# Optimization experiments

Measured on AMD Instinct MI355X. Metric: run time of the kernel, lower is better.

The kernel has to match this reference:

```python
import jax, jax.numpy as jnp
import numpy as np

B, T, C = 4, 2048, 768
H = 12
D = C // H  # head dim 64

def setup_inputs() -> dict:
    key = jax.random.key(0)
    ks = jax.random.split(key, 6)
    scale = 1.0 / np.sqrt(C)
    x = jax.random.normal(ks[0], (B, T, C), dtype=jnp.float32)
    attention_mask = jax.random.randint(ks[1], (B, T), 0, 2, dtype=jnp.int64)
    Wqkv = jax.random.normal(ks[2], (C, 3 * C), dtype=jnp.float32) * scale
    bqkv = jax.random.normal(ks[3], (3 * C,), dtype=jnp.float32) * 0.02
    Wo = jax.random.normal(ks[4], (C, C), dtype=jnp.float32) * scale
    bo = jax.random.normal(ks[5], (C,), dtype=jnp.float32) * 0.02
    return {"x": x, "attention_mask": attention_mask, "Wqkv": Wqkv,
            "bqkv": bqkv, "Wo": Wo, "bo": bo}

def reference(x, attention_mask, Wqkv, bqkv, Wo, bo):
    # fused QKV projection: [B,T,3C]
    qkv = jnp.einsum('btc,cd->btd', x, Wqkv) + bqkv
    q, k, v = jnp.split(qkv, 3, axis=-1)
    # reshape to [B,H,T,D]
    q = q.reshape(B, T, H, D).transpose(0, 2, 1, 3)
    k = k.reshape(B, T, H, D).transpose(0, 2, 1, 3)
    v = v.reshape(B, T, H, D).transpose(0, 2, 1, 3)
    # module quirk: True (attended) where attention_mask == 0
    keep = (attention_mask == 0)[:, None, None, :]  # [B,1,1,T]
    scores = jnp.einsum('bhqd,bhkd->bhqk', q, k) / np.sqrt(D)
    scores = jnp.where(keep, scores, jnp.finfo(scores.dtype).min)
    probs = jax.nn.softmax(scores, axis=-1)
    context = jnp.einsum('bhqk,bhkd->bhqd', probs, v)
    context = context.transpose(0, 2, 1, 3).reshape(B, T, C)
    return jnp.einsum('btc,cd->btd', context, Wo) + bo
```

## Files before the change

### kernel.cpp

```cpp
#include <hip/hip_runtime.h>
#include <stdint.h>

#define AS1 __attribute__((address_space(1)))
#define AS3 __attribute__((address_space(3)))

typedef _Float16 f16;
typedef _Float16 f16x8 __attribute__((ext_vector_type(8)));
typedef _Float16 f16x4 __attribute__((ext_vector_type(4)));
typedef _Float16 f16x2 __attribute__((ext_vector_type(2)));
typedef float    f32x4  __attribute__((ext_vector_type(4)));
typedef float    f32x16 __attribute__((ext_vector_type(16)));
typedef uint32_t u32x4  __attribute__((ext_vector_type(4)));
typedef uint32_t u32x2  __attribute__((ext_vector_type(2)));

#define B_  4
#define T_  2048
#define C_  768
#define H_  12
#define D_  64
#define M_  (B_*T_)
#define N1_ (3*C_)

__device__ __forceinline__ void g2l16(const void* g, void* l) {
  __builtin_amdgcn_global_load_lds((const AS1 void*)g, (AS3 void*)l, 16, 0, 0);
}

__device__ __forceinline__ f32x4 fzero4() { f32x4 z = {0.f, 0.f, 0.f, 0.f}; return z; }

__device__ __forceinline__ uint32_t pk_u32(float a, float b) {
  auto t = __builtin_amdgcn_cvt_pkrtz(a, b);
  return *(uint32_t*)&t;
}

__device__ __forceinline__ void pl32swap(uint32_t& d, uint32_t& s) {
  u32x2 r = __builtin_amdgcn_permlane32_swap(d, s, false, false);
  d = r[0]; s = r[1];
}

__global__ __launch_bounds__(256)
void prep_kernel(const float* __restrict__ Wqkv, f16* __restrict__ WqkvT,
                 const float* __restrict__ Wo, f16* __restrict__ WoT,
                 const float* __restrict__ x, f16* __restrict__ xh,
                 int* __restrict__ idx, int* __restrict__ cnt) {
  __shared__ float tile[32][33];
  const int blk = blockIdx.x;
  if (blk < 2304) {
    const float* in; f16* out; int R, C, bx, by;
    if (blk < 1728) { in = Wqkv; out = WqkvT; R = 768; C = 2304; bx = blk % 72; by = blk / 72; }
    else { const int k = blk - 1728; in = Wo; out = WoT; R = 768; C = 768; bx = k % 24; by = k / 24; }
    const int tx = threadIdx.x & 31, ty = threadIdx.x >> 5;
    const int c0 = bx * 32, r0 = by * 32;
#pragma unroll
    for (int i = 0; i < 32; i += 8)
      tile[ty + i][tx] = in[(long)(r0 + ty + i) * C + c0 + tx];
    __syncthreads();
#pragma unroll
    for (int i = 0; i < 32; i += 8)
      out[(long)(c0 + ty + i) * R + r0 + tx] = (f16)tile[tx][ty + i];
  } else if (blk < 8448) {
    const int i = ((blk - 2304) * 256 + threadIdx.x) * 4;
    const float4 v = *(const float4*)(x + i);
    f16x4 o = {(f16)v.x, (f16)v.y, (f16)v.z, (f16)v.w};
    *(f16x4*)(xh + i) = o;
  } else {
    const int g = (blk - 8448) * 256 + threadIdx.x;
    idx[g] = 0;
    if (g < B_) cnt[g] = 0;
  }
}

__global__ __launch_bounds__(256)
void compact_kernel(const int* __restrict__ mask, int* __restrict__ idx,
                    int* __restrict__ cnt) {
  const int b = blockIdx.y;
  const int t = blockIdx.x * 256 + threadIdx.x;
  if (mask[b * T_ + t] == 0) {
    const int s = atomicAdd(&cnt[b], 1);
    idx[b * T_ + s] = t;
  }
}

template <typename OutT>
__global__ __launch_bounds__(256)
void gemm_bias_kernel(const f16* __restrict__ A, const f16* __restrict__ Bt,
                      const float* __restrict__ bias, OutT* __restrict__ Cc,
                      int K, int ldc) {
  __shared__ f16 lA[128 * 32];
  __shared__ f16 lB[128 * 32];
  const int tid = threadIdx.x;
  const int n0 = blockIdx.x * 128, m0 = blockIdx.y * 128;
  const int lane = tid & 63, w = tid >> 6;
  const int wm = (w & 1) * 64, wn = (w >> 1) * 64;
  const int r15 = lane & 15, q4 = lane >> 4;

  const int c0 = tid, c1 = 256 + tid;
  const int ar0 = c0 >> 2, ak0 = (c0 & 3) * 8;
  const int ar1 = c1 >> 2, ak1 = (c1 & 3) * 8;
  const f16* Ab = A + (long)m0 * K;
  const f16* Bb = Bt + (long)n0 * K;

  f32x4 acc[4][4];
#pragma unroll
  for (int i = 0; i < 4; i++)
#pragma unroll
    for (int j = 0; j < 4; j++) acc[i][j] = fzero4();

  for (int kb = 0; kb < K; kb += 32) {
    g2l16(Ab + (long)ar0 * K + kb + ak0, &lA[c0 * 8]);
    g2l16(Ab + (long)ar1 * K + kb + ak1, &lA[c1 * 8]);
    g2l16(Bb + (long)ar0 * K + kb + ak0, &lB[c0 * 8]);
    g2l16(Bb + (long)ar1 * K + kb + ak1, &lB[c1 * 8]);
    __syncthreads();
    f16x8 af[4], bfv[4];
#pragma unroll
    for (int mi = 0; mi < 4; mi++)
      af[mi] = *(const f16x8*)&lA[(wm + mi * 16 + r15) * 32 + q4 * 8];
#pragma unroll
    for (int ni = 0; ni < 4; ni++)
      bfv[ni] = *(const f16x8*)&lB[(wn + ni * 16 + r15) * 32 + q4 * 8];
#pragma unroll
    for (int mi = 0; mi < 4; mi++)
#pragma unroll
      for (int ni = 0; ni < 4; ni++)
        acc[mi][ni] = __builtin_amdgcn_mfma_f32_16x16x32_f16(af[mi], bfv[ni], acc[mi][ni], 0, 0, 0);
    __syncthreads();
  }

#pragma unroll
  for (int ni = 0; ni < 4; ni++) {
    const int col = n0 + wn + ni * 16 + r15;
    const float bs = bias[col];
#pragma unroll
    for (int mi = 0; mi < 4; mi++) {
#pragma unroll
      for (int r = 0; r < 4; r++) {
        const int row = m0 + wm + mi * 16 + q4 * 4 + r;
        Cc[(long)row * ldc + col] = (OutT)(acc[mi][ni][r] + bs);
      }
    }
  }
}

__global__ __launch_bounds__(512, 2)
void gemm_qkv256(const f16* __restrict__ A, const f16* __restrict__ Bt,
                 const float* __restrict__ bias, f16* __restrict__ Qb,
                 f16* __restrict__ Kc, f16* __restrict__ Vt,
                 const int* __restrict__ idx, const int* __restrict__ cnt) {
  const int K = C_;
  __shared__ f16 lA[2 * 256 * 64];
  __shared__ f16 lB[2 * 256 * 64];
  const int tid = threadIdx.x;
  const int nb = blockIdx.x;
  const int mb = blockIdx.y;
  const bool isQ = nb < 3;

  int b = 0, s0 = 0;
  if (!isQ) {
    b = mb >> 3;
    s0 = (mb & 7) * 256;
    if (s0 >= cnt[b]) return;
  }

  const int lane = tid & 63, w = tid >> 6;
  const int wmi = w >> 2, wni = w & 3;
  const int r15 = lane & 15, q4 = lane >> 4;
  const int rx = (r15 & 7) * 8;

  const int trow = tid >> 3;
  const int koffsw = (((tid & 7) ^ (trow & 7)) * 8);
  const f16* pA[4];
  const f16* pB[4];
#pragma unroll
  for (int i = 0; i < 4; i++) {
    const int ri = i * 64 + trow;
    long grow;
    if (isQ) grow = (long)mb * 256 + ri;
    else     grow = (long)b * T_ + idx[b * T_ + s0 + ri];
    pA[i] = A + grow * K + koffsw;
    pB[i] = Bt + (long)(nb * 256 + ri) * K + koffsw;
  }
  const int lofs = tid * 8;

  f32x4 acc[8][4];
#pragma unroll
  for (int i = 0; i < 8; i++)
#pragma unroll
    for (int j = 0; j < 4; j++) acc[i][j] = fzero4();

#define STAGE_QKV(bufsel, kb) do {                                        \
  const int lb = (bufsel) * 16384;                                        \
  _Pragma("unroll")                                                       \
  for (int i = 0; i < 4; i++) {                                           \
    g2l16(pA[i] + (kb), &lA[lb + i * 4096 + lofs]);                       \
    g2l16(pB[i] + (kb), &lB[lb + i * 4096 + lofs]);                       \
  }                                                                       \
} while (0)

#define COMPUTE_QKV(bufsel) do {                                          \
  const int lb = (bufsel) * 16384;                                        \
  _Pragma("unroll")                                                       \
  for (int kh = 0; kh < 2; kh++) {                                        \
    const int cofs = (kh * 32 + q4 * 8) ^ rx;                             \
    f16x8 af[8], bf[4];                                                   \
    _Pragma("unroll")                                                     \
    for (int mi = 0; mi < 8; mi++)                                        \
      af[mi] = *(const f16x8*)&lA[lb + (wmi * 128 + mi * 16 + r15) * 64 + cofs]; \
    _Pragma("unroll")                                                     \
    for (int ni = 0; ni < 4; ni++)                                        \
      bf[ni] = *(const f16x8*)&lB[lb + (wni * 64 + ni * 16 + r15) * 64 + cofs];  \
    _Pragma("unroll")                                                     \
    for (int mi = 0; mi < 8; mi++)                                        \
      _Pragma("unroll")                                                   \
      for (int ni = 0; ni < 4; ni++)                                      \
        acc[mi][ni] = __builtin_amdgcn_mfma_f32_16x16x32_f16(af[mi], bf[ni], acc[mi][ni], 0, 0, 0); \
  }                                                                       \
} while (0)

  STAGE_QKV(0, 0);
  __syncthreads();

  int cur = 0;
  const int NT = K / 64;
  for (int t = 0; t < NT - 1; t++) {
    STAGE_QKV(cur ^ 1, (t + 1) * 64);
    COMPUTE_QKV(cur);
    __syncthreads();
    cur ^= 1;
  }
  COMPUTE_QKV(cur);

#undef STAGE_QKV
#undef COMPUTE_QKV

#pragma unroll
  for (int ni = 0; ni < 4; ni++) {
    const int cN = nb * 256 + wni * 64 + ni * 16 + r15;
    const float bs = bias[cN];
    if (isQ) {
#pragma unroll
      for (int mi = 0; mi < 8; mi++)
#pragma unroll
        for (int r = 0; r < 4; r++) {
          const long row = (long)mb * 256 + wmi * 128 + mi * 16 + q4 * 4 + r;
          Qb[row * C_ + cN] = (f16)(acc[mi][ni][r] + bs);
        }
    } else if (cN < 2 * C_) {
      const int ocol = cN - C_;
#pragma unroll
      for (int mi = 0; mi < 8; mi++)
#pragma unroll
        for (int r = 0; r < 4; r++) {
          const long row = (long)b * T_ + s0 + wmi * 128 + mi * 16 + q4 * 4 + r;
          Kc[row * C_ + ocol] = (f16)(acc[mi][ni][r] + bs);
        }
    } else {
      const int vcol = cN - 2 * C_;
      const int vh = vcol >> 6, d = vcol & 63;
      f16* dst = Vt + ((long)(b * H_ + vh) * D_ + d) * T_;
#pragma unroll
      for (int mi = 0; mi < 8; mi++) {
        const long slot = s0 + wmi * 128 + mi * 16 + q4 * 4;
        f16x4 v4;
#pragma unroll
        for (int r = 0; r < 4; r++) v4[r] = (f16)(acc[mi][ni][r] + bs);
        *(f16x4*)&dst[slot] = v4;
      }
    }
  }
}

__global__ __launch_bounds__(256, 4)
void attn_kernel(const f16* __restrict__ Qb, const f16* __restrict__ Kc,
                 const f16* __restrict__ vtc, const int* __restrict__ cnt,
                 f16* __restrict__ ctx) {
  __shared__ f16 Ks[2][64 * 64];
  __shared__ f16 Vs[2][64 * 64];
  __shared__ float Ls[4][32];
  const int tid = threadIdx.x, lane = tid & 63, w = tid >> 6;
  const int l31 = lane & 31, hh = lane >> 5;

  const int g = blockIdx.y * 16 + blockIdx.x;
  const int xcd = g & 7, local = g >> 3;
  const int bh = xcd * 6 + (local >> 4);
  const int q0 = (local & 15) * 128;
  const int b = bh / H_, h = bh % H_;

  const f16* Qg = Qb + (long)(b * T_ + q0) * C_ + h * D_;
  const f16* Kbase = Kc + (long)b * T_ * C_ + h * D_;
  const f16* Vg = vtc + (long)bh * D_ * T_;
  const int nk = cnt[b];
  const int nkt = (nk + 63) >> 6;

  const f16 qsc = (f16)0.18033688f;
  f16x8 bq[4];
#pragma unroll
  for (int j = 0; j < 4; j++) {
    f16x8 v = *(const f16x8*)(Qg + (long)(w * 32 + l31) * C_ + j * 16 + hh * 8);
#pragma unroll
    for (int e = 0; e < 8; e++) v[e] = v[e] * qsc;
    bq[j] = v;
  }

  const int r_0 = w * 16 + (lane >> 3);
  const int sc = ((lane & 7) ^ (r_0 & 7)) * 8;
  const f16* Ksrc0 = Kbase + (long)r_0 * C_ + sc;
  const f16* Ksrc1 = Kbase + (long)(r_0 + 8) * C_ + sc;
  const f16* Vsrc0 = Vg + (long)r_0 * T_ + sc;
  const f16* Vsrc1 = Vg + (long)(r_0 + 8) * T_ + sc;
  const int ld0 = w * 1024 + lane * 8;
  const int ld1 = ld0 + 512;

#define ATTN_STAGE(bs, kt) do {                                  \
    g2l16(Ksrc0 + (long)(kt) * C_, &Ks[bs][ld0]);                \
    g2l16(Ksrc1 + (long)(kt) * C_, &Ks[bs][ld1]);                \
    g2l16(Vsrc0 + (kt), &Vs[bs][ld0]);                           \
    g2l16(Vsrc1 + (kt), &Vs[bs][ld1]);                           \
  } while (0)

  float l_acc = 0.f;
  f32x16 O[2];
#pragma unroll
  for (int dt = 0; dt < 2; dt++)
#pragma unroll
    for (int r = 0; r < 16; r++) O[dt][r] = 0.f;

  const int swz = l31 & 7;

  ATTN_STAGE(0, 0);
  __syncthreads();

  int cur = 0;
  for (int t = 0; t < nkt; t++) {
    const int kt = t * 64;
    if (t + 1 < nkt) ATTN_STAGE(cur ^ 1, kt + 64);

    u32x4 paw[4];
    const bool full = (kt + 64 <= nk);
#pragma unroll
    for (int t2 = 0; t2 < 2; t2++) {
      f32x16 acc;
      if (full) {
#pragma unroll
        for (int r = 0; r < 16; r++) acc[r] = 0.f;
      } else {
        const int kbase = kt + t2 * 32 + hh * 4;
#pragma unroll
        for (int g4 = 0; g4 < 4; g4++)
#pragma unroll
          for (int i = 0; i < 4; i++)
            acc[4 * g4 + i] = (kbase + 8 * g4 + i < nk) ? 0.f : -1e30f;
      }
      __builtin_amdgcn_s_setprio(1);
#pragma unroll
      for (int j = 0; j < 4; j++) {
        f16x8 ak = *(const f16x8*)&Ks[cur][(t2 * 32 + l31) * 64 + (((j * 2 + hh) ^ swz) << 3)];
        acc = __builtin_amdgcn_mfma_f32_32x32x16_f16(ak, bq[j], acc, 0, 0, 0);
      }
      __builtin_amdgcn_s_setprio(0);
      uint32_t wg[4], xg[4];
#pragma unroll
      for (int g4 = 0; g4 < 4; g4++) {
        const float p0 = __builtin_amdgcn_exp2f(acc[4 * g4 + 0]);
        const float p1 = __builtin_amdgcn_exp2f(acc[4 * g4 + 1]);
        const float p2 = __builtin_amdgcn_exp2f(acc[4 * g4 + 2]);
        const float p3 = __builtin_amdgcn_exp2f(acc[4 * g4 + 3]);
        l_acc += (p0 + p1) + (p2 + p3);
        wg[g4] = pk_u32(p0, p1);
        xg[g4] = pk_u32(p2, p3);
      }
#pragma unroll
      for (int jl = 0; jl < 2; jl++) {
        uint32_t w0 = wg[2 * jl], w2v = wg[2 * jl + 1];
        uint32_t w1 = xg[2 * jl], w3v = xg[2 * jl + 1];
        pl32swap(w0, w2v);
        pl32swap(w1, w3v);
        paw[2 * t2 + jl][0] = w0;  paw[2 * t2 + jl][1] = w1;
        paw[2 * t2 + jl][2] = w2v; paw[2 * t2 + jl][3] = w3v;
      }
    }

    __builtin_amdgcn_s_setprio(1);
#pragma unroll
    for (int j = 0; j < 4; j++) {
      const f16x8 pa = *(const f16x8*)&paw[j];
#pragma unroll
      for (int dt = 0; dt < 2; dt++) {
        const int vrow = dt * 32 + l31;
        f16x8 vb = *(const f16x8*)&Vs[cur][vrow * 64 + (((j * 2 + hh) ^ swz) << 3)];
        O[dt] = __builtin_amdgcn_mfma_f32_32x32x16_f16(pa, vb, O[dt], 0, 0, 0);
      }
    }
    __builtin_amdgcn_s_setprio(0);

    __syncthreads();
    cur ^= 1;
  }
#undef ATTN_STAGE

  l_acc += __shfl_xor(l_acc, 32);
  asm volatile("s_waitcnt lgkmcnt(0)" ::: "memory");
  if (hh == 0) Ls[w][l31] = l_acc;
  asm volatile("s_waitcnt lgkmcnt(0)" ::: "memory");
#pragma unroll
  for (int g4 = 0; g4 < 4; g4++) {
    const f32x4 lv = *(const f32x4*)&Ls[w][g4 * 8 + hh * 4];
#pragma unroll
    for (int i = 0; i < 4; i++) {
      const float inv = 1.f / lv[i];
      const int row = b * T_ + q0 + w * 32 + g4 * 8 + hh * 4 + i;
#pragma unroll
      for (int dt = 0; dt < 2; dt++)
        ctx[(long)row * C_ + h * D_ + dt * 32 + l31] = (f16)(O[dt][4 * g4 + i] * inv);
    }
  }
}

extern "C" void kernel_launch(void* const* d_in, const int* in_sizes, int n_in,
                              void* d_out, int out_size, void* d_ws, size_t ws_size,
                              hipStream_t stream) {
  (void)in_sizes; (void)n_in; (void)out_size; (void)ws_size;
  const float* x    = (const float*)d_in[0];
  const int*   mask = (const int*)  d_in[1];
  const float* Wqkv = (const float*)d_in[2];
  const float* bqkv = (const float*)d_in[3];
  const float* Wo   = (const float*)d_in[4];
  const float* bo   = (const float*)d_in[5];
  float* out = (float*)d_out;

  char* ws = (char*)d_ws;
  const size_t OFF_WQKVT = 0;
  const size_t OFF_WOT   = OFF_WQKVT + 3538944;
  const size_t OFF_Q     = OFF_WOT + 1179648;
  const size_t OFF_KC    = OFF_Q + 12582912;
  const size_t OFF_VT    = OFF_KC + 12582912;
  const size_t OFF_XH    = OFF_VT + 12582912;
  const size_t OFF_IDX   = OFF_XH + 12582912;
  const size_t OFF_CNT   = OFF_IDX + 32768;
  f16* WqkvT = (f16*)(ws + OFF_WQKVT);
  f16* WoT   = (f16*)(ws + OFF_WOT);
  f16* Qb    = (f16*)(ws + OFF_Q);
  f16* Kc    = (f16*)(ws + OFF_KC);
  f16* Vtc   = (f16*)(ws + OFF_VT);
  f16* xh    = (f16*)(ws + OFF_XH);
  f16* ctx   = (f16*)(ws + OFF_XH);
  int* idx   = (int*)(ws + OFF_IDX);
  int* cnt   = (int*)(ws + OFF_CNT);

  prep_kernel<<<dim3(8480), 256, 0, stream>>>(Wqkv, WqkvT, Wo, WoT, x, xh, idx, cnt);
  compact_kernel<<<dim3(T_ / 256, B_), 256, 0, stream>>>(mask, idx, cnt);
  gemm_qkv256<<<dim3(9, 32), 512, 0, stream>>>(xh, WqkvT, bqkv, Qb, Kc, Vtc, idx, cnt);
  attn_kernel<<<dim3(16, 48), 256, 0, stream>>>(Qb, Kc, Vtc, cnt, ctx);
  gemm_bias_kernel<float><<<dim3(6, 64), 256, 0, stream>>>(ctx, WoT, bo, out, 768, 768);
}
```

Measured before the change: 190.4 us.

## Load K and V fragments directly from global into registers in attention

Removes the LDS double-buffered staging of K and V tiles in the attention kernel. Each wave now reads its MFMA operand fragments straight from global memory (relying on L1/L2 for reuse across the four waves), which drops the per-tile __syncthreads and LDS traffic. Occupancy hint is lowered to 3 blocks per CU to allow more registers for the fragments. The cost is four times redundant global/cache reads per block and no explicit prefetch overlap, so load latency is exposed unless the compiler hoists the loads.

```diff
diff --git a/kernel.cpp b/kernel.cpp
--- a/kernel.cpp
+++ b/kernel.cpp
@@ -7,7 +7,6 @@
 typedef _Float16 f16;
 typedef _Float16 f16x8 __attribute__((ext_vector_type(8)));
 typedef _Float16 f16x4 __attribute__((ext_vector_type(4)));
-typedef _Float16 f16x2 __attribute__((ext_vector_type(2)));
 typedef float    f32x4  __attribute__((ext_vector_type(4)));
 typedef float    f32x16 __attribute__((ext_vector_type(16)));
 typedef uint32_t u32x4  __attribute__((ext_vector_type(4)));
@@ -269,12 +268,10 @@
   }
 }
 
-__global__ __launch_bounds__(256, 4)
+__global__ __launch_bounds__(256, 3)
 void attn_kernel(const f16* __restrict__ Qb, const f16* __restrict__ Kc,
                  const f16* __restrict__ vtc, const int* __restrict__ cnt,
                  f16* __restrict__ ctx) {
-  __shared__ f16 Ks[2][64 * 64];
-  __shared__ f16 Vs[2][64 * 64];
   __shared__ float Ls[4][32];
   const int tid = threadIdx.x, lane = tid & 63, w = tid >> 6;
   const int l31 = lane & 31, hh = lane >> 5;
@@ -286,8 +283,6 @@
   const int b = bh / H_, h = bh % H_;
 
   const f16* Qg = Qb + (long)(b * T_ + q0) * C_ + h * D_;
-  const f16* Kbase = Kc + (long)b * T_ * C_ + h * D_;
-  const f16* Vg = vtc + (long)bh * D_ * T_;
   const int nk = cnt[b];
   const int nkt = (nk + 63) >> 6;
 
@@ -301,21 +296,9 @@
     bq[j] = v;
   }
 
-  const int r_0 = w * 16 + (lane >> 3);
-  const int sc = ((lane & 7) ^ (r_0 & 7)) * 8;
-  const f16* Ksrc0 = Kbase + (long)r_0 * C_ + sc;
-  const f16* Ksrc1 = Kbase + (long)(r_0 + 8) * C_ + sc;
-  const f16* Vsrc0 = Vg + (long)r_0 * T_ + sc;
-  const f16* Vsrc1 = Vg + (long)(r_0 + 8) * T_ + sc;
-  const int ld0 = w * 1024 + lane * 8;
-  const int ld1 = ld0 + 512;
-
-#define ATTN_STAGE(bs, kt) do {                                  \
-    g2l16(Ksrc0 + (long)(kt) * C_, &Ks[bs][ld0]);                \
-    g2l16(Ksrc1 + (long)(kt) * C_, &Ks[bs][ld1]);                \
-    g2l16(Vsrc0 + (kt), &Vs[bs][ld0]);                           \
-    g2l16(Vsrc1 + (kt), &Vs[bs][ld1]);                           \
-  } while (0)
+  const f16* Kl = Kc + ((long)b * T_ + l31) * C_ + h * D_ + hh * 8;
+  const f16* Vl0 = vtc + ((long)bh * D_ + l31) * T_ + hh * 8;
+  const f16* Vl1 = Vl0 + 32 * T_;
 
   float l_acc = 0.f;
   f32x16 O[2];
@@ -324,15 +307,16 @@
 #pragma unroll
     for (int r = 0; r < 16; r++) O[dt][r] = 0.f;
 
-  const int swz = l31 & 7;
-
-  ATTN_STAGE(0, 0);
-  __syncthreads();
-
-  int cur = 0;
   for (int t = 0; t < nkt; t++) {
     const int kt = t * 64;
-    if (t + 1 < nkt) ATTN_STAGE(cur ^ 1, kt + 64);
+    const f16* Kt = Kl + (long)kt * C_;
+
+    f16x8 ak[2][4];
+#pragma unroll
+    for (int t2 = 0; t2 < 2; t2++)
+#pragma unroll
+      for (int j = 0; j < 4; j++)
+        ak[t2][j] = *(const f16x8*)(Kt + (long)(t2 * 32) * C_ + j * 16);
 
     u32x4 paw[4];
     const bool full = (kt + 64 <= nk);
@@ -352,10 +336,8 @@
       }
       __builtin_amdgcn_s_setprio(1);
 #pragma unroll
-      for (int j = 0; j < 4; j++) {
-        f16x8 ak = *(const f16x8*)&Ks[cur][(t2 * 32 + l31) * 64 + (((j * 2 + hh) ^ swz) << 3)];
-        acc = __builtin_amdgcn_mfma_f32_32x32x16_f16(ak, bq[j], acc, 0, 0, 0);
-      }
+      for (int j = 0; j < 4; j++)
+        acc = __builtin_amdgcn_mfma_f32_32x32x16_f16(ak[t2][j], bq[j], acc, 0, 0, 0);
       __builtin_amdgcn_s_setprio(0);
       uint32_t wg[4], xg[4];
 #pragma unroll
@@ -379,26 +361,23 @@
       }
     }
 
+    f16x8 vf[4][2];
+#pragma unroll
+    for (int j = 0; j < 4; j++) {
+      vf[j][0] = *(const f16x8*)(Vl0 + kt + j * 16);
+      vf[j][1] = *(const f16x8*)(Vl1 + kt + j * 16);
+    }
     __builtin_amdgcn_s_setprio(1);
 #pragma unroll
     for (int j = 0; j < 4; j++) {
       const f16x8 pa = *(const f16x8*)&paw[j];
-#pragma unroll
-      for (int dt = 0; dt < 2; dt++) {
-        const int vrow = dt * 32 + l31;
-        f16x8 vb = *(const f16x8*)&Vs[cur][vrow * 64 + (((j * 2 + hh) ^ swz) << 3)];
-        O[dt] = __builtin_amdgcn_mfma_f32_32x32x16_f16(pa, vb, O[dt], 0, 0, 0);
-      }
+      O[0] = __builtin_amdgcn_mfma_f32_32x32x16_f16(pa, vf[j][0], O[0], 0, 0, 0);
+      O[1] = __builtin_amdgcn_mfma_f32_32x32x16_f16(pa, vf[j][1], O[1], 0, 0, 0);
     }
     __builtin_amdgcn_s_setprio(0);
-
-    __syncthreads();
-    cur ^= 1;
-  }
-#undef ATTN_STAGE
+  }
 
   l_acc += __shfl_xor(l_acc, 32);
-  asm volatile("s_waitcnt lgkmcnt(0)" ::: "memory");
   if (hh == 0) Ls[w][l31] = l_acc;
   asm volatile("s_waitcnt lgkmcnt(0)" ::: "memory");
 #pragma unroll
```

After: 247.5 us. 1.3x slower.

## Double-buffer LDS and swizzle tiles in bias GEMM kernel

Applied to the files above, without the earlier changes.

The generic bias GEMM now uses two LDS buffers so the async global-to-LDS loads for the next K tile are issued before computing the current one, dropping one barrier per iteration. LDS column chunks are XOR-swizzled by row to reduce bank conflicts on the fragment reads. It doubles the LDS footprint, which may lower occupancy.

```diff
diff --git a/kernel.cpp b/kernel.cpp
--- a/kernel.cpp
+++ b/kernel.cpp
@@ -7,7 +7,6 @@
 typedef _Float16 f16;
 typedef _Float16 f16x8 __attribute__((ext_vector_type(8)));
 typedef _Float16 f16x4 __attribute__((ext_vector_type(4)));
-typedef _Float16 f16x2 __attribute__((ext_vector_type(2)));
 typedef float    f32x4  __attribute__((ext_vector_type(4)));
 typedef float    f32x16 __attribute__((ext_vector_type(16)));
 typedef uint32_t u32x4  __attribute__((ext_vector_type(4)));
@@ -85,19 +84,20 @@
 void gemm_bias_kernel(const f16* __restrict__ A, const f16* __restrict__ Bt,
                       const float* __restrict__ bias, OutT* __restrict__ Cc,
                       int K, int ldc) {
-  __shared__ f16 lA[128 * 32];
-  __shared__ f16 lB[128 * 32];
+  __shared__ f16 lA[2 * 128 * 32];
+  __shared__ f16 lB[2 * 128 * 32];
   const int tid = threadIdx.x;
   const int n0 = blockIdx.x * 128, m0 = blockIdx.y * 128;
   const int lane = tid & 63, w = tid >> 6;
   const int wm = (w & 1) * 64, wn = (w >> 1) * 64;
   const int r15 = lane & 15, q4 = lane >> 4;
-
-  const int c0 = tid, c1 = 256 + tid;
-  const int ar0 = c0 >> 2, ak0 = (c0 & 3) * 8;
-  const int ar1 = c1 >> 2, ak1 = (c1 & 3) * 8;
-  const f16* Ab = A + (long)m0 * K;
-  const f16* Bb = Bt + (long)n0 * K;
+  const int rkey = (r15 >> 1) & 3;
+
+  const int r0 = tid >> 2, jj = tid & 3;
+  const int scol = (jj ^ ((r0 >> 1) & 3)) * 8;
+  const f16* pA0 = A + (long)(m0 + r0) * K + scol;
+  const f16* pB0 = Bt + (long)(n0 + r0) * K + scol;
+  const long rstep = (long)64 * K;
 
   f32x4 acc[4][4];
 #pragma unroll
@@ -105,26 +105,46 @@
 #pragma unroll
     for (int j = 0; j < 4; j++) acc[i][j] = fzero4();
 
-  for (int kb = 0; kb < K; kb += 32) {
-    g2l16(Ab + (long)ar0 * K + kb + ak0, &lA[c0 * 8]);
-    g2l16(Ab + (long)ar1 * K + kb + ak1, &lA[c1 * 8]);
-    g2l16(Bb + (long)ar0 * K + kb + ak0, &lB[c0 * 8]);
-    g2l16(Bb + (long)ar1 * K + kb + ak1, &lB[c1 * 8]);
+#define STAGE_WO(bufsel, kb) do {                                   \
+  const int lb = (bufsel) * 4096;                                   \
+  g2l16(pA0 + (kb), &lA[lb + tid * 8]);                             \
+  g2l16(pA0 + rstep + (kb), &lA[lb + 2048 + tid * 8]);              \
+  g2l16(pB0 + (kb), &lB[lb + tid * 8]);                             \
+  g2l16(pB0 + rstep + (kb), &lB[lb + 2048 + tid * 8]);              \
+} while (0)
+
+#define COMPUTE_WO(bufsel) do {                                     \
+  const int lb = (bufsel) * 4096;                                   \
+  const int cofs = (q4 ^ rkey) * 8;                                 \
+  f16x8 af[4], bfv[4];                                              \
+  _Pragma("unroll")                                                 \
+  for (int mi = 0; mi < 4; mi++)                                    \
+    af[mi] = *(const f16x8*)&lA[lb + (wm + mi * 16 + r15) * 32 + cofs]; \
+  _Pragma("unroll")                                                 \
+  for (int ni = 0; ni < 4; ni++)                                    \
+    bfv[ni] = *(const f16x8*)&lB[lb + (wn + ni * 16 + r15) * 32 + cofs]; \
+  _Pragma("unroll")                                                 \
+  for (int mi = 0; mi < 4; mi++)                                    \
+    _Pragma("unroll")                                               \
+    for (int ni = 0; ni < 4; ni++)                                  \
+      acc[mi][ni] = __builtin_amdgcn_mfma_f32_16x16x32_f16(af[mi], bfv[ni], acc[mi][ni], 0, 0, 0); \
+} while (0)
+
+  STAGE_WO(0, 0);
+  __syncthreads();
+
+  int cur = 0;
+  const int NT = K / 32;
+  for (int t = 0; t < NT - 1; t++) {
+    STAGE_WO(cur ^ 1, (t + 1) * 32);
+    COMPUTE_WO(cur);
     __syncthreads();
-    f16x8 af[4], bfv[4];
-#pragma unroll
-    for (int mi = 0; mi < 4; mi++)
-      af[mi] = *(const f16x8*)&lA[(wm + mi * 16 + r15) * 32 + q4 * 8];
-#pragma unroll
-    for (int ni = 0; ni < 4; ni++)
-      bfv[ni] = *(const f16x8*)&lB[(wn + ni * 16 + r15) * 32 + q4 * 8];
-#pragma unroll
-    for (int mi = 0; mi < 4; mi++)
-#pragma unroll
-      for (int ni = 0; ni < 4; ni++)
-        acc[mi][ni] = __builtin_amdgcn_mfma_f32_16x16x32_f16(af[mi], bfv[ni], acc[mi][ni], 0, 0, 0);
-    __syncthreads();
-  }
+    cur ^= 1;
+  }
+  COMPUTE_WO(cur);
+
+#undef STAGE_WO
+#undef COMPUTE_WO
 
 #pragma unroll
   for (int ni = 0; ni < 4; ni++) {
```

After: 187.9 us. No clear change (-1.3%).
